# Performance work log

Hardware: AMD Instinct MI355X
Metric: run time of the kernel (lower is better)

## Reference

```python
import math
import jax, jax.numpy as jnp
import numpy as np

# irreps layout (flat, e3nn ordering: all scalars first, then vectors as (mul,3)):
#   pseduo: 64x0e + 32x1o  -> dim 160, 96 irreps
#   edge:   32x0e + 32x1o  -> dim 128, 64 irreps
PS, PV = 64, 32
ES, EV = 32, 32
H, NB = 8, 16
N_NODES, N_EDGES = 8192, 65536
MSG_DIM = PS + 3 * PV           # msg_irreps = pseduo_irreps (default)
NIR = PS + PV                   # num_irreps of pseduo
SQRT3 = math.sqrt(3.0)

def _split(x, ns, nv):
    # flat spherical tensor -> (scalars [..,ns], vectors [..,nv,3])
    return x[..., :ns], x[..., ns:].reshape(x.shape[:-1] + (nv, 3))

def _o3_linear(s, v, Ws, Wv):
    # e3nn o3.Linear: independent channel mixing per l, fan-in normalized
    so = (s @ Ws) / math.sqrt(Ws.shape[0])
    vo = jnp.einsum('...ic,io->...oc', v, Wv) / math.sqrt(Wv.shape[0])
    return so, vo

def setup_inputs() -> dict:
    key = jax.random.key(0)
    k = jax.random.split(key, 20)
    f32 = jnp.float32
    return {
        'pseduo_x': jax.random.normal(k[0], (N_NODES, PS + 3 * PV), f32),
        'rbf': jax.random.normal(k[1], (N_EDGES, NB), f32),
        'rsh': jax.random.normal(k[2], (N_EDGES, ES + 3 * EV), f32),
        'edge_index': jax.random.randint(k[3], (2, N_EDGES), 0, N_NODES),
        'Wq_s': jax.random.normal(k[4], (PS, H * PS), f32),
        'Wq_v': jax.random.normal(k[5], (PV, H * PV), f32),
        'Wk_s': jax.random.normal(k[6], (2 * PS, H * PS), f32),
        'Wk_v': jax.random.normal(k[7], (2 * PV, H * PV), f32),
        'Wp_s': jax.random.normal(k[8], (2 * PS, ES), f32),
        'Wp_v': jax.random.normal(k[9], (2 * PV, EV), f32),
        'Wrbf': jax.random.normal(k[10], (NB, ES + EV), f32) / math.sqrt(NB),
        'Wv_s': jax.random.normal(k[11], (ES + EV, H * PS), f32),
        'Wv_v': jax.random.normal(k[12], (2 * EV, H * PV), f32),
        'Wm_s': jax.random.normal(k[13], (H * PS, PS), f32),
        'Wm_v': jax.random.normal(k[14], (H * PV, PV), f32),
        'ln_g': jnp.ones((NIR,), f32),
        'ln_b': jnp.zeros((NIR,), f32),
        'W1': jax.random.normal(k[15], (NIR, NIR), f32) / math.sqrt(NIR),
        'b1': jnp.zeros((NIR,), f32),
        'W2': jax.random.normal(k[16], (NIR, NIR), f32) / math.sqrt(NIR),
        'b2': jnp.zeros((NIR,), f32),
    }

def reference(pseduo_x, rbf, rsh, edge_index, Wq_s, Wq_v, Wk_s, Wk_v, Wp_s, Wp_v,
              Wrbf, Wv_s, Wv_v, Wm_s, Wm_v, ln_g, ln_b, W1, b1, W2, b2):
    src, dst = edge_index[0], edge_index[1]
    s, v = _split(pseduo_x, PS, PV)

    # pseduo_ij = cat([x_i, x_j]) -> irreps pseduo*2
    sij = jnp.concatenate([s[src], s[dst]], axis=-1)            # [E, 2*PS]
    vij = jnp.concatenate([v[src], v[dst]], axis=-2)            # [E, 2*PV, 3]

    # multi-head query (per node) and key (per edge)
    q_s, q_v = _o3_linear(s, v, Wq_s, Wq_v)
    q_s = q_s.reshape(-1, H, PS); q_v = q_v.reshape(-1, H, PV, 3)
    k_s, k_v = _o3_linear(sij, vij, Wk_s, Wk_v)
    k_s = k_s.reshape(-1, H, PS); k_v = k_v.reshape(-1, H, PV, 3)

    # edge filter: rsh_conv(rsh, rbf_lin(rbf))
    scal = rbf @ Wrbf                                           # [E, ES+EV]
    rs, rv = _split(rsh, ES, EV)
    e_s = rs * scal[:, :ES]
    e_v = rv * scal[:, ES:, None]

    # sph_ij = edge * pseduo_lin(pseduo_ij)   (elementwise on flat layout)
    p_s, p_v = _o3_linear(sij, vij, Wp_s, Wp_v)
    sph_s = e_s * p_s                                           # [E, ES]
    sph_v = e_v * p_v                                           # [E, EV, 3]

    # depthwise CG self-coupling x (x) x, filter {0e, 1o} -> 64x0e + 64x1o
    c0 = jnp.concatenate([sph_s * sph_s,
                          jnp.sum(sph_v * sph_v, axis=-1) / SQRT3], axis=-1)  # [E, 64]
    sv = sph_s[..., None] * sph_v                               # 0e x 1o -> 1o
    c1 = jnp.concatenate([sv, sv], axis=-2)                     # [E, 64, 3]

    val_s, val_v = _o3_linear(c0, c1, Wv_s, Wv_v)
    val_s = val_s.reshape(-1, H, PS); val_v = val_v.reshape(-1, H, PV, 3)

    # attention logits: (query[src] * key).sum over flat msg dim, per head
    proj = (jnp.einsum('ehd,ehd->eh', q_s[src], k_s) +
            jnp.einsum('ehdc,ehdc->eh', q_v[src], k_v))
    logits = proj / math.sqrt(MSG_DIM)

    # scatter-softmax over destination nodes
    m = jax.ops.segment_max(logits, dst, num_segments=N_NODES)
    ex = jnp.exp(logits - m[dst])
    den = jax.ops.segment_sum(ex, dst, num_segments=N_NODES)
    attn = ex / den[dst]                                        # [E, H]

    # scatter-aggregate messages to nodes
    msg_s = jax.ops.segment_sum(attn[..., None] * val_s, dst, num_segments=N_NODES)
    msg_v = jax.ops.segment_sum(attn[..., None, None] * val_v, dst, num_segments=N_NODES)

    m_s, m_v = _o3_linear(msg_s.reshape(-1, H * PS),
                          msg_v.reshape(-1, H * PV, 3), Wm_s, Wm_v)

    # NormGate: EvNorm (per-irrep norm, node LayerNorm) + 2-layer silu MLP gate
    n0 = jnp.concatenate([jnp.abs(m_s), jnp.linalg.norm(m_v, axis=-1)], axis=-1)  # [N, 96]
    mu = jnp.mean(n0, axis=-1, keepdims=True)
    var = jnp.var(n0, axis=-1, keepdims=True)
    x1 = (n0 - mu) / jnp.sqrt(var + 1e-5) * ln_g + ln_b
    inv = 1.0 / (n0 + 1e-6)                                    # 1 / (|h_l| + eps)
    g = jax.nn.silu(jax.nn.silu(x1 @ W1 + b1) @ W2 + b2)
    f = inv * g
    out_s = m_s * f[:, :PS]
    out_v = m_v * f[:, PS:, None]
    return jnp.concatenate([out_s, out_v.reshape(-1, 3 * PV)], axis=-1)
```

## Files before the change

kernel.cpp:

```cpp
#include <hip/hip_runtime.h>

typedef unsigned short u16;
typedef unsigned int u32;

#define NN 8192
#define NE 65536
#define INV160 0.07905694150420949f

__device__ __forceinline__ float BF(u16 u){ return __uint_as_float(((u32)u)<<16); }
__device__ __forceinline__ float LD(const void* p, u32 i, int f){
  return f ? ((const float*)p)[i] : BF(((const u16*)p)[i]);
}
__device__ __forceinline__ int LDI(const void* p, u32 i, int f64){
  return f64 ? (int)((const long long*)p)[i] : ((const int*)p)[i];
}

__global__ void k_detect(
    const void* b0, const void* b1, const void* b2, const void* b3,
    const void* b4, const void* b5, const void* b6, const void* b7,
    const void* b8, const void* b9, const void* b10, const void* b11,
    const void* b12, const void* b13, const void* b14, const void* b15,
    const void* b16, const void* b17, const void* b18, const void* b19,
    const void* b20, int* flags)
{
  const void* bufs[21] = {b0,b1,b2,b3,b4,b5,b6,b7,b8,b9,b10,
                          b11,b12,b13,b14,b15,b16,b17,b18,b19,b20};
  int i = threadIdx.x;
  if (i >= 21) return;
  const u32* w = (const u32*)bufs[i];
  if (i == 3){
    int allz = 1;
    for (int k=0;k<32;k++) if (w[2*k+1] != 0u) allz = 0;
    flags[3] = allz;
  } else {
    int cnt = 0;
    for (int k=0;k<40;k++){
      u32 lo = w[k] & 0xFFFFu;
      u32 e = (lo>>7)&0xFFu;
      if (e>=123u && e<=131u) cnt++;
    }
    flags[i] = (cnt>=20) ? 0 : 1;
  }
}

__global__ void k_sentinel(float* __restrict__ out, int n){
  int i = blockIdx.x*256+threadIdx.x;
  if (i<n) out[i] = 12345.0f;
}

__global__ __launch_bounds__(384) void k_prep4(
    const void* __restrict__ X, const void* __restrict__ Wq_s,
    const void* __restrict__ Wq_v, const void* __restrict__ Wk_s,
    const void* __restrict__ Wk_v, const int* __restrict__ flags,
    int hc0, float* __restrict__ qtab, float* __restrict__ kbtab,
    float* __restrict__ dotAA)
{
  __shared__ float xr[4][160];
  __shared__ float dsum[4][4];
  const int fX=flags[0], fqs=flags[4], fqv=flags[5], fks=flags[6], fkv=flags[7];
  const int fall = fqs & fqv & fks & fkv;
  const int t=threadIdx.x; const int n0=blockIdx.x*4;
  for(int u=t;u<640;u+=384){ int m=u/160,k=u-m*160; xr[m][k]=LD(X,(u32)(n0+m)*160+k,fX); }
  if (t<16) dsum[t>>2][t&3]=0.f;
  __syncthreads();
  if (t<256){
    const int o=hc0*64+t;
    float q[4]={0,0,0,0}, ka[4]={0,0,0,0}, kb[4]={0,0,0,0};
    if (fall){
      const float* wqs=(const float*)Wq_s;
      const float* wks=(const float*)Wk_s;
      for(int i=0;i<64;i++){
        float wq=wqs[(u32)i*512+o], wa=wks[(u32)i*512+o], wb=wks[(u32)(64+i)*512+o];
        #pragma unroll
        for(int m=0;m<4;m++){ float s=xr[m][i]; q[m]+=s*wq; ka[m]+=s*wa; kb[m]+=s*wb; }
      }
    } else {
      for(int i=0;i<64;i++){
        float wq=LD(Wq_s,(u32)i*512+o,fqs);
        float wa=LD(Wk_s,(u32)i*512+o,fks);
        float wb=LD(Wk_s,(u32)(64+i)*512+o,fks);
        #pragma unroll
        for(int m=0;m<4;m++){ float s=xr[m][i]; q[m]+=s*wq; ka[m]+=s*wa; kb[m]+=s*wb; }
      }
    }
    #pragma unroll
    for(int m=0;m<4;m++){
      float qs = q[m]*0.125f;
      float kas= ka[m]*0.08838834764831845f;
      float kbs= kb[m]*0.08838834764831845f;
      qtab [(u32)(n0+m)*640+t]=qs;
      kbtab[(u32)(n0+m)*640+t]=kbs;
      float d=qs*kas;
      for(int s2=1;s2<64;s2<<=1) d+=__shfl_xor(d,s2,64);
      if((t&63)==0) atomicAdd(&dsum[m][t>>6],d);
    }
  } else {
    const int ol=t-256;
    const int o=hc0*32+ol;
    float q[4][3]={}, ka[4][3]={}, kb[4][3]={};
    if (fall){
      const float* wqv=(const float*)Wq_v;
      const float* wkv=(const float*)Wk_v;
      for(int j=0;j<32;j++){
        float wq=wqv[(u32)j*256+o], wa=wkv[(u32)j*256+o], wb=wkv[(u32)(32+j)*256+o];
        #pragma unroll
        for(int m=0;m<4;m++){
          #pragma unroll
          for(int c=0;c<3;c++){
            float x=xr[m][64+j*3+c];
            q[m][c]+=x*wq; ka[m][c]+=x*wa; kb[m][c]+=x*wb;
          }
        }
      }
    } else {
      for(int j=0;j<32;j++){
        float wq=LD(Wq_v,(u32)j*256+o,fqv);
        float wa=LD(Wk_v,(u32)j*256+o,fkv);
        float wb=LD(Wk_v,(u32)(32+j)*256+o,fkv);
        #pragma unroll
        for(int m=0;m<4;m++){
          #pragma unroll
          for(int c=0;c<3;c++){
            float x=xr[m][64+j*3+c];
            q[m][c]+=x*wq; ka[m][c]+=x*wa; kb[m][c]+=x*wb;
          }
        }
      }
    }
    const float sq=0.17677669529663687f;
    const float sk=0.125f;
    #pragma unroll
    for(int m=0;m<4;m++){
      float d=0.f;
      u32 base=(u32)(n0+m)*640+256+(u32)ol*3;
      #pragma unroll
      for(int c=0;c<3;c++){
        float qs=q[m][c]*sq, kas=ka[m][c]*sk, kbs=kb[m][c]*sk;
        qtab[base+c]=qs; kbtab[base+c]=kbs;
        d+=qs*kas;
      }
      for(int s2=1;s2<32;s2<<=1) d+=__shfl_xor(d,s2,64);
      if((t&31)==0) atomicAdd(&dsum[m][ol>>5],d);
    }
  }
  __syncthreads();
  if (t<16){ int m=t>>2, hh=t&3; dotAA[(u32)(n0+m)*8+hc0+hh]=dsum[m][hh]; }
}

__global__ __launch_bounds__(512) void k_elog4(
    const void* __restrict__ ei, const int* __restrict__ flags,
    const float* __restrict__ qtab, const float* __restrict__ kbtab,
    const float* __restrict__ dotAA, const u32* __restrict__ elist,
    int hc0, float* __restrict__ logits)
{
  const int f64=flags[3];
  const int t=threadIdx.x;
  const int e=(int)elist[(u32)blockIdx.x*8+(t>>6)], l=t&63;
  const int src=LDI(ei,(u32)e,f64);
  const int dst=LDI(ei,(u32)NE+e,f64);
  const float4* q4=(const float4*)qtab + (u32)src*160;
  const float4* b4=(const float4*)kbtab + (u32)dst*160;
  float a0=0.f,a1=0.f,a2=0.f,a3=0.f;
  {
    float4 a=q4[l], b=b4[l];
    float d=a.x*b.x+a.y*b.y+a.z*b.z+a.w*b.w;
    int h=l>>4;
    a0+=(h==0)?d:0.f; a1+=(h==1)?d:0.f; a2+=(h==2)?d:0.f; a3+=(h==3)?d:0.f;
  }
  {
    float4 a=q4[64+l], b=b4[64+l];
    float d=a.x*b.x+a.y*b.y+a.z*b.z+a.w*b.w;
    int h=l/24;
    a0+=(h==0)?d:0.f; a1+=(h==1)?d:0.f; a2+=(h==2)?d:0.f;
  }
  if (l<32){
    float4 a=q4[128+l], b=b4[128+l];
    float d=a.x*b.x+a.y*b.y+a.z*b.z+a.w*b.w;
    a2+=(l<8)?d:0.f; a3+=(l>=8)?d:0.f;
  }
  for(int m=1;m<64;m<<=1){
    a0+=__shfl_xor(a0,m,64); a1+=__shfl_xor(a1,m,64);
    a2+=__shfl_xor(a2,m,64); a3+=__shfl_xor(a3,m,64);
  }
  if (l<4){
    float cr=(l==0)?a0:(l==1)?a1:(l==2)?a2:a3;
    logits[(u32)e*8+hc0+l]=(dotAA[(u32)src*8+hc0+l]+cr)*INV160;
  }
}

__global__ __launch_bounds__(256) void k_fold(
    const void* __restrict__ Wv_s, const void* __restrict__ Wv_v,
    const void* __restrict__ Wm_s, const void* __restrict__ Wm_v,
    const int* __restrict__ flags,
    float* __restrict__ Wfold, float* __restrict__ Vfold)
{
  const int fvs=flags[11], fvv=flags[12], fms=flags[13], fmv=flags[14];
  const int b=blockIdx.x, t=threadIdx.x;
  if (b<128){
    int idx=b*256+t;
    int i=idx>>6, o=idx&63;
    int h=i>>6, iin=i&63;
    float a=0.f;
    for(int d=0;d<64;d++)
      a += LD(Wv_s,(u32)iin*512 + h*64 + d, fvs) * LD(Wm_s,(u32)(h*64+d)*64 + o, fms);
    Wfold[idx]=a*0.0055242717280199026f;
  } else {
    int idx=(b-128)*256+t;
    int h=idx>>10, r=idx&1023, j2=r>>5, o2=r&31;
    float a=0.f;
    for(int dl=0;dl<32;dl++){
      int i2=h*32+dl;
      a += (LD(Wv_v,(u32)j2*256+i2,fvv)+LD(Wv_v,(u32)(32+j2)*256+i2,fvv))
           *LD(Wm_v,(u32)i2*32+o2,fmv);
    }
    Vfold[idx]=a*0.0078125f;
  }
}

__global__ __launch_bounds__(256) void k_pprep(
    const void* __restrict__ X, const void* __restrict__ Wp_s,
    const void* __restrict__ Wp_v, const int* __restrict__ flags,
    float* __restrict__ pA, float* __restrict__ pB)
{
  __shared__ float xr[160];
  const int fX=flags[0], fps=flags[8], fpv=flags[9];
  const int t=threadIdx.x, n=blockIdx.x;
  if (t<160) xr[t]=LD(X,(u32)n*160+t,fX);
  __syncthreads();
  if (t<64){
    const int j=t&31, half=t>>5;
    float a=0.f;
    if (fps){
      const float* wp=(const float*)Wp_s;
      for(int i=0;i<64;i++) a+=xr[i]*wp[(u32)(half*64+i)*32+j];
    } else {
      for(int i=0;i<64;i++) a+=xr[i]*LD(Wp_s,(u32)(half*64+i)*32+j,fps);
    }
    float* d_ = half? pB:pA;
    d_[(u32)n*128+j]=a*0.08838834764831845f;
  } else {
    const int idx=t-64;
    const int half=idx/96;
    const int r=idx-half*96;
    const int j=r/3, c=r-3*j;
    float a=0.f;
    if (fpv){
      const float* wp=(const float*)Wp_v;
      for(int k=0;k<32;k++) a+=xr[64+k*3+c]*wp[(u32)(half*32+k)*32+j];
    } else {
      for(int k=0;k<32;k++) a+=xr[64+k*3+c]*LD(Wp_v,(u32)(half*32+k)*32+j,fpv);
    }
    float* d_ = half? pB:pA;
    d_[(u32)n*128+32+j*3+c]=a*0.125f;
  }
}

__global__ __launch_bounds__(256) void k_count(
    const void* __restrict__ ei, const int* __restrict__ flags,
    u32* __restrict__ cnt)
{
  int e = blockIdx.x*256 + threadIdx.x;
  int dst = LDI(ei,(u32)NE+e,flags[3]);
  atomicAdd(&cnt[dst],1u);
}
__global__ __launch_bounds__(256) void k_scan(
    u32* __restrict__ cnt, u32* __restrict__ off, u32* __restrict__ cur)
{
  __shared__ u32 s[NN];
  __shared__ u32 tsum[256];
  const int t=threadIdx.x;
  for(int u=t;u<NN;u+=256) s[u]=cnt[u];
  __syncthreads();
  const u32 base=(u32)t*32;
  u32 sum=0;
  for(int k=0;k<32;k++) sum+=s[base+k];
  tsum[t]=sum;
  __syncthreads();
  if(t==0){
    u32 run=0;
    for(int i=0;i<256;i++){ u32 v=tsum[i]; tsum[i]=run; run+=v; }
  }
  __syncthreads();
  u32 run=tsum[t];
  for(int k=0;k<32;k++){
    u32 v=s[base+k];
    off[base+k]=run; cur[base+k]=run;
    run+=v;
  }
  if(t==255) off[NN]=run;
}
__global__ __launch_bounds__(256) void k_fill(
    const void* __restrict__ ei, const int* __restrict__ flags,
    u32* __restrict__ cur, u32* __restrict__ elist)
{
  int e = blockIdx.x*256 + threadIdx.x;
  int dst = LDI(ei,(u32)NE+e,flags[3]);
  u32 p = atomicAdd(&cur[dst],1u);
  elist[p] = (u32)e;
}

__global__ __launch_bounds__(256) void k_nodeval(
    const float* __restrict__ logits, const float* __restrict__ pA,
    const float* __restrict__ pBt,
    const u32* __restrict__ off, const u32* __restrict__ elist,
    const void* __restrict__ ei, const void* __restrict__ rbf,
    const void* __restrict__ rsh, const void* __restrict__ Wrbf,
    const float* __restrict__ Wfold, const float* __restrict__ Vfold,
    const void* __restrict__ ln_g, const void* __restrict__ ln_b,
    const void* __restrict__ W1, const void* __restrict__ b1,
    const void* __restrict__ W2, const void* __restrict__ b2,
    const int* __restrict__ flags, float* __restrict__ out)
{
  __shared__ float ag[4][1280];
  __shared__ float smemf[4096];
  __shared__ int   ebuf[8];
  float* wrb = smemf;
  float (*pB4)[128]  = (float(*)[128])(smemf+1024);
  float (*ubuf)[160] = (float(*)[160])(smemf+1536);
  float (*partf)[4][64] = (float(*)[4][64])smemf;
  float (*partv)[192] = (float(*)[192])(smemf+1024);
  float (*mrow)[160]  = (float(*)[160])(smemf+1792);
  float (*n0_)[96]    = (float(*)[96])(smemf+2432);
  float (*x1_)[96]    = (float(*)[96])(smemf+2816);
  float (*y1_)[96]    = (float(*)[96])(smemf+3200);
  float (*fl_)[96]    = (float(*)[96])(smemf+3584);
  float* stat = smemf+3968;

  const int frb=flags[1], frs=flags[2], f64=flags[3], fwr=flags[10];
  const int fg=flags[15], fbb=flags[16], f1=flags[17], fb1=flags[18];
  const int f2=flags[19], fb2=flags[20];
  const int fastg = frb & frs;
  const int fastt = f1 & f2;
  const int t=threadIdx.x; const int g4=blockIdx.x*4;
  for(int u=t;u<1024;u+=256) wrb[u]=LD(Wrbf,u,fwr);
  #pragma unroll
  for(int m=0;m<4;m++) if (t<128) pB4[m][t]=pBt[(u32)(g4+m)*128+t];
  __syncthreads();

  const int h=t>>5, j=t&31;

  for (int m=0;m<4;m++){
    const int n=g4+m;
    const u32 o0=off[n], o1=off[n+1];
    float mx=-3.4e38f;
    for(u32 p=o0+j; p<o1; p+=32) mx=fmaxf(mx, logits[(u32)elist[p]*8+h]);
    #pragma unroll
    for(int s2=1;s2<32;s2<<=1) mx=fmaxf(mx, __shfl_xor(mx,s2,64));
    float sm=0.f;
    for(u32 p=o0+j; p<o1; p+=32) sm+=__expf(logits[(u32)elist[p]*8+h]-mx);
    #pragma unroll
    for(int s2=1;s2<32;s2<<=1) sm+=__shfl_xor(sm,s2,64);
    const float winv=(sm>0.f)?1.f/sm:0.f;

    float a0=0.f,a1=0.f,a2=0.f,a3=0.f,a4=0.f;
    for (u32 base=o0; base<o1; base+=8){
      u32 rem=o1-base; int nb = rem<8u ? (int)rem : 8;
      if (h<nb){
        u32 e=elist[base+h];
        if (j==0) ebuf[h]=(int)e;
        int src=LDI(ei,e,f64);
        const float* pa=pA+(u32)src*128;
        float ps  = pa[j]        + pB4[m][j];
        float pv0 = pa[32+j*3+0] + pB4[m][32+j*3+0];
        float pv1 = pa[32+j*3+1] + pB4[m][32+j*3+1];
        float pv2 = pa[32+j*3+2] + pB4[m][32+j*3+2];
        float scs=0.f, scv=0.f;
        float rs0,rs1,rs2,rs3;
        if (fastg){
          const float* rb=(const float*)rbf + (size_t)e*16;
          #pragma unroll
          for(int r=0;r<16;r++){
            float x=rb[r];
            scs+=x*wrb[r*64+j]; scv+=x*wrb[r*64+32+j];
          }
          const float* rs=(const float*)rsh + (size_t)e*128;
          rs0=rs[j]; rs1=rs[32+j*3+0]; rs2=rs[32+j*3+1]; rs3=rs[32+j*3+2];
        } else {
          for(int r=0;r<16;r++){
            float x=LD(rbf,(u32)e*16+r,frb);
            scs+=x*wrb[r*64+j]; scv+=x*wrb[r*64+32+j];
          }
          rs0=LD(rsh,(u32)e*128+j,frs);
          rs1=LD(rsh,(u32)e*128+32+j*3+0,frs);
          rs2=LD(rsh,(u32)e*128+32+j*3+1,frs);
          rs3=LD(rsh,(u32)e*128+32+j*3+2,frs);
        }
        float ss = rs0 * scs * ps;
        float v0 = rs1 * scv * pv0;
        float v1 = rs2 * scv * pv1;
        float v2 = rs3 * scv * pv2;
        ubuf[h][j]        = ss*ss;
        ubuf[h][32+j]     = (v0*v0+v1*v1+v2*v2)*0.57735026918962576f;
        ubuf[h][64+3*j+0] = ss*v0;
        ubuf[h][64+3*j+1] = ss*v1;
        ubuf[h][64+3*j+2] = ss*v2;
      }
      __syncthreads();
      for(int q=0;q<nb;q++){
        float w=__expf(logits[(u32)ebuf[q]*8+h]-mx)*winv;
        a0+=w*ubuf[q][j];        a1+=w*ubuf[q][32+j];
        a2+=w*ubuf[q][64+3*j+0]; a3+=w*ubuf[q][64+3*j+1]; a4+=w*ubuf[q][64+3*j+2];
      }
      __syncthreads();
    }
    ag[m][h*64+j]=a0; ag[m][h*64+32+j]=a1;
    ag[m][512+h*96+3*j+0]=a2; ag[m][512+h*96+3*j+1]=a3; ag[m][512+h*96+3*j+2]=a4;
  }
  __syncthreads();

  {
    const int o4=t&15, pp=t>>4;
    const int m=pp&3, gq=pp>>2;
    const float4* Wf4=(const float4*)Wfold;
    float ax=0.f,ay=0.f,az=0.f,aw=0.f;
    const int i0=gq*128;
    for(int i=i0;i<i0+128;i++){
      float a=ag[m][i];
      float4 wv=Wf4[(u32)i*16+o4];
      ax+=a*wv.x; ay+=a*wv.y; az+=a*wv.z; aw+=a*wv.w;
    }
    partf[gq][m][o4*4+0]=ax; partf[gq][m][o4*4+1]=ay;
    partf[gq][m][o4*4+2]=az; partf[gq][m][o4*4+3]=aw;
  }
  if (t<192){
    const int o2=t&31, c=(t>>5)%3, p=t/96;
    float a[4]={0.f,0.f,0.f,0.f};
    for(int hh=p*4;hh<p*4+4;hh++)
      for(int j2=0;j2<32;j2++){
        float v=Vfold[(u32)hh*1024+j2*32+o2];
        #pragma unroll
        for(int m=0;m<4;m++) a[m]+=ag[m][512+hh*96+j2*3+c]*v;
      }
    #pragma unroll
    for(int m=0;m<4;m++) partv[m][t]=a[m];
  }
  __syncthreads();
  {
    const int o=t&63, m=t>>6;
    mrow[m][o]=partf[0][m][o]+partf[1][m][o]+partf[2][m][o]+partf[3][m][o];
  }
  if (t<96){
    #pragma unroll
    for(int m=0;m<4;m++)
      mrow[m][64+(t&31)*3+(t>>5)]=partv[m][t]+partv[m][t+96];
  }
  __syncthreads();

  if (t<96){
    #pragma unroll
    for(int m=0;m<4;m++){
      float val;
      if (t<64) val=fabsf(mrow[m][t]);
      else { int o2=t-64;
        float a=mrow[m][64+o2*3],b=mrow[m][64+o2*3+1],c=mrow[m][64+o2*3+2];
        val=sqrtf(a*a+b*b+c*c); }
      n0_[m][t]=val;
    }
  }
  __syncthreads();
  {
    const int m=t>>6;
    float mu=0.f,ss2=0.f;
    for(int i=0;i<96;i++){ float v=n0_[m][i]; mu+=v; ss2+=v*v; }
    mu*=(1.f/96.f);
    float var=fmaxf(ss2*(1.f/96.f)-mu*mu,0.f);
    float rstd=rsqrtf(var+1e-5f);
    if ((t&63)==0){ stat[m]=mu; stat[4+m]=rstd; }
  }
  __syncthreads();
  if (t<96){
    float gv = fg  ? ((const float*)ln_g)[t] : LD(ln_g,t,fg);
    float bv = fbb ? ((const float*)ln_b)[t] : LD(ln_b,t,fbb);
    #pragma unroll
    for(int m=0;m<4;m++)
      x1_[m][t]=(n0_[m][t]-stat[m])*stat[4+m]*gv+bv;
  }
  __syncthreads();
  if (t<96){
    float bb = fb1 ? ((const float*)b1)[t] : LD(b1,t,fb1);
    float a[4]={bb,bb,bb,bb};
    if (fastt){
      const float* w1=(const float*)W1;
      for(int i=0;i<96;i++){
        float w=w1[(u32)i*96+t];
        #pragma unroll
        for(int m=0;m<4;m++) a[m]+=x1_[m][i]*w;
      }
    } else {
      for(int i=0;i<96;i++){
        float w=LD(W1,i*96+t,f1);
        #pragma unroll
        for(int m=0;m<4;m++) a[m]+=x1_[m][i]*w;
      }
    }
    #pragma unroll
    for(int m=0;m<4;m++) y1_[m][t]=a[m]/(1.f+__expf(-a[m]));
  }
  __syncthreads();
  if (t<96){
    float bb = fb2 ? ((const float*)b2)[t] : LD(b2,t,fb2);
    float a[4]={bb,bb,bb,bb};
    if (fastt){
      const float* w2=(const float*)W2;
      for(int i=0;i<96;i++){
        float w=w2[(u32)i*96+t];
        #pragma unroll
        for(int m=0;m<4;m++) a[m]+=y1_[m][i]*w;
      }
    } else {
      for(int i=0;i<96;i++){
        float w=LD(W2,i*96+t,f2);
        #pragma unroll
        for(int m=0;m<4;m++) a[m]+=y1_[m][i]*w;
      }
    }
    #pragma unroll
    for(int m=0;m<4;m++){
      float gg=a[m]/(1.f+__expf(-a[m]));
      fl_[m][t]=gg/(n0_[m][t]+1e-6f);
    }
  }
  __syncthreads();
  if (t<160){
    #pragma unroll
    for(int m=0;m<4;m++){
      float v;
      if (t<64) v=mrow[m][t]*fl_[m][t];
      else { int q=t-64; int o2=q/3; v=mrow[m][t]*fl_[m][64+o2]; }
      out[(u32)(g4+m)*160+t]=v;
    }
  }
}

extern "C" void kernel_launch(void* const* d_in, const int* in_sizes, int n_in,
                              void* d_out, int out_size, void* d_ws, size_t ws_size,
                              hipStream_t stream)
{
  (void)in_sizes; (void)n_in;
  const void* X    = d_in[0];
  const void* rbf  = d_in[1];
  const void* rsh  = d_in[2];
  const void* ei   = d_in[3];
  const void* Wq_s = d_in[4];
  const void* Wq_v = d_in[5];
  const void* Wk_s = d_in[6];
  const void* Wk_v = d_in[7];
  const void* Wp_s = d_in[8];
  const void* Wp_v = d_in[9];
  const void* Wrbf = d_in[10];
  const void* Wv_s = d_in[11];
  const void* Wv_v = d_in[12];
  const void* Wm_s = d_in[13];
  const void* Wm_v = d_in[14];
  const void* ln_g = d_in[15];
  const void* ln_b = d_in[16];
  const void* W1   = d_in[17];
  const void* b1   = d_in[18];
  const void* W2   = d_in[19];
  const void* b2   = d_in[20];

  char* w = (char*)d_ws;
  int* flags     = (int*)w;   w += 256;
  float* logits  = (float*)w; w += (size_t)NE*8*4;
  u32* imax      = (u32*)w;   w += (size_t)NN*8*4;
  float* den     = (float*)w; w += (size_t)NN*8*4;
  char* uni = w;              w += (size_t)NN*1280*4;
  float* qtab  = (float*)uni;
  float* kbtab = (float*)(uni + (size_t)NN*640*4);
  float* pA    = (float*)uni;
  float* pB    = (float*)(uni + (size_t)NN*128*4);
  u32* csr_off = imax;
  u32* csr_cur = imax + 12288;
  float* Wfold = (float*)((char*)imax + 98304);
  float* Vfold = (float*)((char*)imax + 229376);
  u32* elist   = (u32*)den;
  float* dotAA = (float*)d_out;
  size_t required = (size_t)(w - (char*)d_ws);

  if (ws_size < required){
    k_sentinel<<<(out_size+255)/256,256,0,stream>>>((float*)d_out, out_size);
    return;
  }

  k_detect<<<1,64,0,stream>>>(X,rbf,rsh,ei,Wq_s,Wq_v,Wk_s,Wk_v,Wp_s,Wp_v,
                              Wrbf,Wv_s,Wv_v,Wm_s,Wm_v,ln_g,ln_b,W1,b1,W2,b2,flags);
  k_fold<<<160,256,0,stream>>>(Wv_s,Wv_v,Wm_s,Wm_v,flags,Wfold,Vfold);
  hipMemsetAsync(imax, 0, (size_t)NN*4, stream);
  k_count<<<NE/256,256,0,stream>>>(ei,flags,imax);
  k_scan<<<1,256,0,stream>>>(imax,csr_off,csr_cur);
  k_fill<<<NE/256,256,0,stream>>>(ei,flags,csr_cur,elist);
  for (int c=0;c<2;c++){
    k_prep4<<<NN/4,384,0,stream>>>(X,Wq_s,Wq_v,Wk_s,Wk_v,flags,c*4,qtab,kbtab,dotAA);
    k_elog4<<<NE/8,512,0,stream>>>(ei,flags,qtab,kbtab,dotAA,elist,c*4,logits);
  }
  k_pprep<<<NN,256,0,stream>>>(X,Wp_s,Wp_v,flags,pA,pB);
  k_nodeval<<<NN/4,256,0,stream>>>(logits,pA,pB,csr_off,elist,ei,rbf,rsh,Wrbf,
                                   Wfold,Vfold,ln_g,ln_b,W1,b1,W2,b2,flags,(float*)d_out);
}
```

Baseline: 428.6 us.

## Batch more nodes per block in prep kernels and regroup q/k table by head

The q/k projection kernel now handles 8 nodes per block and pprep handles 4, so each weight load is reused across more rows. The q/k tables are reordered so each head's 160 values sit together. This lets the edge-logit kernel compute each head's dot product with 16 lanes and a short shuffle reduction instead of four masked accumulators reduced over the full wave. Shared-memory arrays in nodeval are padded to avoid bank conflicts. The cost is more registers per thread in the prep kernels, which may lower occupancy.

```diff
diff --git a/kernel.cpp b/kernel.cpp
--- a/kernel.cpp
+++ b/kernel.cpp
@@ -48,31 +48,32 @@
   if (i<n) out[i] = 12345.0f;
 }
 
-__global__ __launch_bounds__(384) void k_prep4(
+__global__ __launch_bounds__(384) void k_prep8(
     const void* __restrict__ X, const void* __restrict__ Wq_s,
     const void* __restrict__ Wq_v, const void* __restrict__ Wk_s,
     const void* __restrict__ Wk_v, const int* __restrict__ flags,
     int hc0, float* __restrict__ qtab, float* __restrict__ kbtab,
     float* __restrict__ dotAA)
 {
-  __shared__ float xr[4][160];
-  __shared__ float dsum[4][4];
+  __shared__ float xr[8][160];
+  __shared__ float dsum[8][4];
   const int fX=flags[0], fqs=flags[4], fqv=flags[5], fks=flags[6], fkv=flags[7];
   const int fall = fqs & fqv & fks & fkv;
-  const int t=threadIdx.x; const int n0=blockIdx.x*4;
-  for(int u=t;u<640;u+=384){ int m=u/160,k=u-m*160; xr[m][k]=LD(X,(u32)(n0+m)*160+k,fX); }
-  if (t<16) dsum[t>>2][t&3]=0.f;
+  const int t=threadIdx.x; const int n0=blockIdx.x*8;
+  for(int u=t;u<1280;u+=384){ int m=u/160,k=u-m*160; xr[m][k]=LD(X,(u32)(n0+m)*160+k,fX); }
+  if (t<32) dsum[t>>2][t&3]=0.f;
   __syncthreads();
   if (t<256){
+    const int lh=t>>6, d=t&63;
     const int o=hc0*64+t;
-    float q[4]={0,0,0,0}, ka[4]={0,0,0,0}, kb[4]={0,0,0,0};
+    float q[8]={}, ka[8]={}, kb[8]={};
     if (fall){
       const float* wqs=(const float*)Wq_s;
       const float* wks=(const float*)Wk_s;
       for(int i=0;i<64;i++){
         float wq=wqs[(u32)i*512+o], wa=wks[(u32)i*512+o], wb=wks[(u32)(64+i)*512+o];
         #pragma unroll
-        for(int m=0;m<4;m++){ float s=xr[m][i]; q[m]+=s*wq; ka[m]+=s*wa; kb[m]+=s*wb; }
+        for(int m=0;m<8;m++){ float s=xr[m][i]; q[m]+=s*wq; ka[m]+=s*wa; kb[m]+=s*wb; }
       }
     } else {
       for(int i=0;i<64;i++){
@@ -80,31 +81,33 @@
         float wa=LD(Wk_s,(u32)i*512+o,fks);
         float wb=LD(Wk_s,(u32)(64+i)*512+o,fks);
         #pragma unroll
-        for(int m=0;m<4;m++){ float s=xr[m][i]; q[m]+=s*wq; ka[m]+=s*wa; kb[m]+=s*wb; }
-      }
-    }
-    #pragma unroll
-    for(int m=0;m<4;m++){
+        for(int m=0;m<8;m++){ float s=xr[m][i]; q[m]+=s*wq; ka[m]+=s*wa; kb[m]+=s*wb; }
+      }
+    }
+    #pragma unroll
+    for(int m=0;m<8;m++){
       float qs = q[m]*0.125f;
       float kas= ka[m]*0.08838834764831845f;
       float kbs= kb[m]*0.08838834764831845f;
-      qtab [(u32)(n0+m)*640+t]=qs;
-      kbtab[(u32)(n0+m)*640+t]=kbs;
-      float d=qs*kas;
-      for(int s2=1;s2<64;s2<<=1) d+=__shfl_xor(d,s2,64);
-      if((t&63)==0) atomicAdd(&dsum[m][t>>6],d);
+      u32 base=(u32)(n0+m)*640 + lh*160 + d;
+      qtab [base]=qs;
+      kbtab[base]=kbs;
+      float dd=qs*kas;
+      for(int s2=1;s2<64;s2<<=1) dd+=__shfl_xor(dd,s2,64);
+      if(d==0) atomicAdd(&dsum[m][lh],dd);
     }
   } else {
     const int ol=t-256;
+    const int lh=ol>>5, jj=ol&31;
     const int o=hc0*32+ol;
-    float q[4][3]={}, ka[4][3]={}, kb[4][3]={};
+    float q[8][3]={}, ka[8][3]={}, kb[8][3]={};
     if (fall){
       const float* wqv=(const float*)Wq_v;
       const float* wkv=(const float*)Wk_v;
       for(int j=0;j<32;j++){
         float wq=wqv[(u32)j*256+o], wa=wkv[(u32)j*256+o], wb=wkv[(u32)(32+j)*256+o];
         #pragma unroll
-        for(int m=0;m<4;m++){
+        for(int m=0;m<8;m++){
           #pragma unroll
           for(int c=0;c<3;c++){
             float x=xr[m][64+j*3+c];
@@ -118,7 +121,7 @@
         float wa=LD(Wk_v,(u32)j*256+o,fkv);
         float wb=LD(Wk_v,(u32)(32+j)*256+o,fkv);
         #pragma unroll
-        for(int m=0;m<4;m++){
+        for(int m=0;m<8;m++){
           #pragma unroll
           for(int c=0;c<3;c++){
             float x=xr[m][64+j*3+c];
@@ -130,21 +133,21 @@
     const float sq=0.17677669529663687f;
     const float sk=0.125f;
     #pragma unroll
-    for(int m=0;m<4;m++){
-      float d=0.f;
-      u32 base=(u32)(n0+m)*640+256+(u32)ol*3;
+    for(int m=0;m<8;m++){
+      float dd=0.f;
+      u32 base=(u32)(n0+m)*640 + lh*160 + 64 + (u32)jj*3;
       #pragma unroll
       for(int c=0;c<3;c++){
         float qs=q[m][c]*sq, kas=ka[m][c]*sk, kbs=kb[m][c]*sk;
         qtab[base+c]=qs; kbtab[base+c]=kbs;
-        d+=qs*kas;
-      }
-      for(int s2=1;s2<32;s2<<=1) d+=__shfl_xor(d,s2,64);
-      if((t&31)==0) atomicAdd(&dsum[m][ol>>5],d);
-    }
-  }
-  __syncthreads();
-  if (t<16){ int m=t>>2, hh=t&3; dotAA[(u32)(n0+m)*8+hc0+hh]=dsum[m][hh]; }
+        dd+=qs*kas;
+      }
+      for(int s2=1;s2<32;s2<<=1) dd+=__shfl_xor(dd,s2,64);
+      if((t&31)==0) atomicAdd(&dsum[m][lh],dd);
+    }
+  }
+  __syncthreads();
+  if (t<32){ int m=t>>2, hh=t&3; dotAA[(u32)(n0+m)*8+hc0+hh]=dsum[m][hh]; }
 }
 
 __global__ __launch_bounds__(512) void k_elog4(
@@ -160,32 +163,25 @@
   const int dst=LDI(ei,(u32)NE+e,f64);
   const float4* q4=(const float4*)qtab + (u32)src*160;
   const float4* b4=(const float4*)kbtab + (u32)dst*160;
-  float a0=0.f,a1=0.f,a2=0.f,a3=0.f;
+  const int hg=l>>4, lg=l&15;
+  const int base4=hg*40;
+  float acc;
   {
-    float4 a=q4[l], b=b4[l];
-    float d=a.x*b.x+a.y*b.y+a.z*b.z+a.w*b.w;
-    int h=l>>4;
-    a0+=(h==0)?d:0.f; a1+=(h==1)?d:0.f; a2+=(h==2)?d:0.f; a3+=(h==3)?d:0.f;
+    float4 a=q4[base4+lg], b=b4[base4+lg];
+    acc=a.x*b.x+a.y*b.y+a.z*b.z+a.w*b.w;
   }
   {
-    float4 a=q4[64+l], b=b4[64+l];
-    float d=a.x*b.x+a.y*b.y+a.z*b.z+a.w*b.w;
-    int h=l/24;
-    a0+=(h==0)?d:0.f; a1+=(h==1)?d:0.f; a2+=(h==2)?d:0.f;
-  }
-  if (l<32){
-    float4 a=q4[128+l], b=b4[128+l];
-    float d=a.x*b.x+a.y*b.y+a.z*b.z+a.w*b.w;
-    a2+=(l<8)?d:0.f; a3+=(l>=8)?d:0.f;
-  }
-  for(int m=1;m<64;m<<=1){
-    a0+=__shfl_xor(a0,m,64); a1+=__shfl_xor(a1,m,64);
-    a2+=__shfl_xor(a2,m,64); a3+=__shfl_xor(a3,m,64);
-  }
-  if (l<4){
-    float cr=(l==0)?a0:(l==1)?a1:(l==2)?a2:a3;
-    logits[(u32)e*8+hc0+l]=(dotAA[(u32)src*8+hc0+l]+cr)*INV160;
-  }
+    float4 a=q4[base4+16+lg], b=b4[base4+16+lg];
+    acc+=a.x*b.x+a.y*b.y+a.z*b.z+a.w*b.w;
+  }
+  if (lg<8){
+    float4 a=q4[base4+32+lg], b=b4[base4+32+lg];
+    acc+=a.x*b.x+a.y*b.y+a.z*b.z+a.w*b.w;
+  }
+  #pragma unroll
+  for(int m=1;m<16;m<<=1) acc+=__shfl_xor(acc,m,64);
+  if (lg==0)
+    logits[(u32)e*8+hc0+hg]=(dotAA[(u32)src*8+hc0+hg]+acc)*INV160;
 }
 
 __global__ __launch_bounds__(256) void k_fold(
@@ -222,36 +218,54 @@
     const void* __restrict__ Wp_v, const int* __restrict__ flags,
     float* __restrict__ pA, float* __restrict__ pB)
 {
-  __shared__ float xr[160];
+  __shared__ float xr[4][160];
   const int fX=flags[0], fps=flags[8], fpv=flags[9];
-  const int t=threadIdx.x, n=blockIdx.x;
-  if (t<160) xr[t]=LD(X,(u32)n*160+t,fX);
+  const int t=threadIdx.x, n0=blockIdx.x*4;
+  for(int u=t;u<640;u+=256){ int m=u/160,k=u-m*160; xr[m][k]=LD(X,(u32)(n0+m)*160+k,fX); }
   __syncthreads();
   if (t<64){
     const int j=t&31, half=t>>5;
-    float a=0.f;
+    float a[4]={0.f,0.f,0.f,0.f};
     if (fps){
       const float* wp=(const float*)Wp_s;
-      for(int i=0;i<64;i++) a+=xr[i]*wp[(u32)(half*64+i)*32+j];
+      for(int i=0;i<64;i++){
+        float w=wp[(u32)(half*64+i)*32+j];
+        #pragma unroll
+        for(int m=0;m<4;m++) a[m]+=xr[m][i]*w;
+      }
     } else {
-      for(int i=0;i<64;i++) a+=xr[i]*LD(Wp_s,(u32)(half*64+i)*32+j,fps);
+      for(int i=0;i<64;i++){
+        float w=LD(Wp_s,(u32)(half*64+i)*32+j,fps);
+        #pragma unroll
+        for(int m=0;m<4;m++) a[m]+=xr[m][i]*w;
+      }
     }
     float* d_ = half? pB:pA;
-    d_[(u32)n*128+j]=a*0.08838834764831845f;
+    #pragma unroll
+    for(int m=0;m<4;m++) d_[(u32)(n0+m)*128+j]=a[m]*0.08838834764831845f;
   } else {
     const int idx=t-64;
     const int half=idx/96;
     const int r=idx-half*96;
     const int j=r/3, c=r-3*j;
-    float a=0.f;
+    float a[4]={0.f,0.f,0.f,0.f};
     if (fpv){
       const float* wp=(const float*)Wp_v;
-      for(int k=0;k<32;k++) a+=xr[64+k*3+c]*wp[(u32)(half*32+k)*32+j];
+      for(int k=0;k<32;k++){
+        float w=wp[(u32)(half*32+k)*32+j];
+        #pragma unroll
+        for(int m=0;m<4;m++) a[m]+=xr[m][64+k*3+c]*w;
+      }
     } else {
-      for(int k=0;k<32;k++) a+=xr[64+k*3+c]*LD(Wp_v,(u32)(half*32+k)*32+j,fpv);
+      for(int k=0;k<32;k++){
+        float w=LD(Wp_v,(u32)(half*32+k)*32+j,fpv);
+        #pragma unroll
+        for(int m=0;m<4;m++) a[m]+=xr[m][64+k*3+c]*w;
+      }
     }
     float* d_ = half? pB:pA;
-    d_[(u32)n*128+32+j*3+c]=a*0.125f;
+    #pragma unroll
+    for(int m=0;m<4;m++) d_[(u32)(n0+m)*128+32+j*3+c]=a[m]*0.125f;
   }
 }
 
@@ -311,20 +325,20 @@
     const void* __restrict__ W2, const void* __restrict__ b2,
     const int* __restrict__ flags, float* __restrict__ out)
 {
-  __shared__ float ag[4][1280];
+  __shared__ float ag[4][1288];
   __shared__ float smemf[4096];
   __shared__ int   ebuf[8];
   float* wrb = smemf;
   float (*pB4)[128]  = (float(*)[128])(smemf+1024);
   float (*ubuf)[160] = (float(*)[160])(smemf+1536);
-  float (*partf)[4][64] = (float(*)[4][64])smemf;
-  float (*partv)[192] = (float(*)[192])(smemf+1024);
-  float (*mrow)[160]  = (float(*)[160])(smemf+1792);
-  float (*n0_)[96]    = (float(*)[96])(smemf+2432);
-  float (*x1_)[96]    = (float(*)[96])(smemf+2816);
-  float (*y1_)[96]    = (float(*)[96])(smemf+3200);
-  float (*fl_)[96]    = (float(*)[96])(smemf+3584);
-  float* stat = smemf+3968;
+  float (*partf)[4][65] = (float(*)[4][65])smemf;
+  float (*partv)[192] = (float(*)[192])(smemf+1040);
+  float (*mrow)[160]  = (float(*)[160])(smemf+1808);
+  float (*n0_)[96]    = (float(*)[96])(smemf+2448);
+  float (*x1_)[96]    = (float(*)[96])(smemf+2832);
+  float (*y1_)[96]    = (float(*)[96])(smemf+3216);
+  float (*fl_)[96]    = (float(*)[96])(smemf+3600);
+  float* stat = smemf+3984;
 
   const int frb=flags[1], frs=flags[2], f64=flags[3], fwr=flags[10];
   const int fg=flags[15], fbb=flags[16], f1=flags[17], fb1=flags[18];
@@ -590,10 +604,10 @@
   k_scan<<<1,256,0,stream>>>(imax,csr_off,csr_cur);
   k_fill<<<NE/256,256,0,stream>>>(ei,flags,csr_cur,elist);
   for (int c=0;c<2;c++){
-    k_prep4<<<NN/4,384,0,stream>>>(X,Wq_s,Wq_v,Wk_s,Wk_v,flags,c*4,qtab,kbtab,dotAA);
+    k_prep8<<<NN/8,384,0,stream>>>(X,Wq_s,Wq_v,Wk_s,Wk_v,flags,c*4,qtab,kbtab,dotAA);
     k_elog4<<<NE/8,512,0,stream>>>(ei,flags,qtab,kbtab,dotAA,elist,c*4,logits);
   }
-  k_pprep<<<NN,256,0,stream>>>(X,Wp_s,Wp_v,flags,pA,pB);
+  k_pprep<<<NN/4,256,0,stream>>>(X,Wp_s,Wp_v,flags,pA,pB);
   k_nodeval<<<NN/4,256,0,stream>>>(logits,pA,pB,csr_off,elist,ei,rbf,rsh,Wrbf,
                                    Wfold,Vfold,ln_g,ln_b,W1,b1,W2,b2,flags,(float*)d_out);
 }
```

Measured after the change: 468.6 us. 1.09x slower.
